# Optimization experiments

Hardware: AMD Instinct MI355X
Metric: run time of the kernel (lower is better)

Reference implementation:

```python
import jax, jax.numpy as jnp
import numpy as np

NUM_NODES = 100000
NUM_EDGES = 625000
IN_FEATURES = 128
OUT_FEATURES = 128


def setup_inputs() -> dict:
    key = jax.random.key(0)
    k1, k2, k3, k4 = jax.random.split(key, 4)
    x = jax.random.normal(k1, (NUM_NODES, IN_FEATURES), dtype=jnp.float32)
    edge_index = jax.random.randint(k2, (2, NUM_EDGES), 0, NUM_NODES, dtype=jnp.int64)
    # Xavier uniform for W (fan_in=IN, fan_out=OUT); B initialized to zeros in the
    # original, but we use small random values so gradients flow through both paths.
    limit = float(np.sqrt(6.0 / (IN_FEATURES + OUT_FEATURES)))
    W = jax.random.uniform(k3, (OUT_FEATURES, IN_FEATURES), dtype=jnp.float32,
                           minval=-limit, maxval=limit)
    B = jax.random.uniform(k4, (OUT_FEATURES, IN_FEATURES), dtype=jnp.float32,
                           minval=-limit, maxval=limit)
    return {"x": x, "edge_index": edge_index, "W": W, "B": B}


def reference(x, edge_index, W, B):
    sources, destinations = edge_index[0], edge_index[1]
    # message: gather destination features, scatter-add into source slots
    messages = x[destinations]                                        # [E, F_in]
    agg = jax.ops.segment_sum(messages, sources, num_segments=x.shape[0])  # [N, F_in]
    # in-degree (w.r.t. sources) normalization; zero-degree -> divide by 1
    deg = jax.ops.segment_sum(jnp.ones((sources.shape[0],), dtype=x.dtype),
                              sources, num_segments=x.shape[0])       # [N]
    deg = jnp.where(deg == 0, jnp.ones_like(deg), deg)
    agg = agg / deg[:, None]
    # update: (W @ messages.T + B @ x.T).T == messages @ W.T + x @ B.T
    out = agg @ W.T + x @ B.T                                         # [N, F_out]
    return out
```

## Files before the change

kernel.cpp:

```cpp
#include <hip/hip_runtime.h>

#define F_IN   128
#define F_OUT  128

typedef __attribute__((ext_vector_type(8))) short short8;
typedef __attribute__((ext_vector_type(4))) float floatx4;

__device__ __forceinline__ float bf16u_to_f_lo(unsigned int u) {
    union { unsigned int i; float f; } c; c.i = u << 16; return c.f;
}
__device__ __forceinline__ float bf16u_to_f_hi(unsigned int u) {
    union { unsigned int i; float f; } c; c.i = u & 0xffff0000u; return c.f;
}
__device__ __forceinline__ unsigned short f_to_bf16(float f) {
    union { float f; unsigned int i; } c; c.f = f;
    unsigned int u = c.i;
    u += 0x7fffu + ((u >> 16) & 1u);
    return (unsigned short)(u >> 16);
}
__device__ __forceinline__ unsigned int pack2(unsigned short a, unsigned short b) {
    return (unsigned int)a | ((unsigned int)b << 16);
}

__global__ void zero_kernel(int* __restrict__ p, long n) {
    long i = (long)blockIdx.x * blockDim.x + threadIdx.x;
    long stride = (long)gridDim.x * blockDim.x;
    for (; i < n; i += stride) p[i] = 0;
}

__global__ void hist_kernel(const int* __restrict__ src, int* __restrict__ cnt, int E) {
    int e = blockIdx.x * blockDim.x + threadIdx.x;
    if (e < E) atomicAdd(&cnt[src[e]], 1);
}

__global__ __launch_bounds__(256) void chunk_sums_kernel(const int* __restrict__ cnt,
                                                         int* __restrict__ partials, int n) {
    __shared__ int s[256];
    int b = blockIdx.x, t = threadIdx.x;
    int base = b * 1024 + t * 4;
    int sum = 0;
#pragma unroll
    for (int j = 0; j < 4; ++j) {
        int i = base + j;
        if (i < n) sum += cnt[i];
    }
    s[t] = sum;
    __syncthreads();
    for (int d = 128; d > 0; d >>= 1) {
        if (t < d) s[t] += s[t + d];
        __syncthreads();
    }
    if (t == 0) partials[b] = s[0];
}

__global__ __launch_bounds__(128) void scan_partials_kernel(const int* __restrict__ partials,
                                                            int* __restrict__ chunk_off, int nch) {
    __shared__ int s[128];
    int t = threadIdx.x;
    s[t] = (t < nch) ? partials[t] : 0;
    __syncthreads();
    for (int d = 1; d < 128; d <<= 1) {
        int val = s[t];
        int add = (t >= d) ? s[t - d] : 0;
        __syncthreads();
        s[t] = val + add;
        __syncthreads();
    }
    if (t < nch) chunk_off[t] = (t > 0) ? s[t - 1] : 0;
}

__global__ __launch_bounds__(256) void scan_chunks_kernel(int* __restrict__ off,
                                                          const int* __restrict__ chunk_off,
                                                          int n) {
    __shared__ int s[256];
    int b = blockIdx.x, t = threadIdx.x;
    int base = b * 1024 + t * 4;
    int v[4];
#pragma unroll
    for (int j = 0; j < 4; ++j) {
        int i = base + j;
        v[j] = (i < n) ? off[i] : 0;
    }
    int l1 = v[0], l2 = l1 + v[1], l3 = l2 + v[2], tot = l3 + v[3];
    s[t] = tot;
    __syncthreads();
    for (int d = 1; d < 256; d <<= 1) {
        int val = s[t];
        int add = (t >= d) ? s[t - d] : 0;
        __syncthreads();
        s[t] = val + add;
        __syncthreads();
    }
    int thr_excl = ((t > 0) ? s[t - 1] : 0) + chunk_off[b];
    if (base + 0 < n) off[base + 0] = thr_excl;
    if (base + 1 < n) off[base + 1] = thr_excl + l1;
    if (base + 2 < n) off[base + 2] = thr_excl + l2;
    if (base + 3 < n) off[base + 3] = thr_excl + l3;
}

__global__ void fill_kernel(const int* __restrict__ ei, int* __restrict__ off,
                            int* __restrict__ dst_sorted, int E) {
    int e = blockIdx.x * blockDim.x + threadIdx.x;
    if (e < E) {
        int s = ei[e];
        int d = ei[E + e];
        int p = atomicAdd(&off[s], 1);
        dst_sorted[p] = d;
    }
}

__global__ __launch_bounds__(256) void convert_x_kernel(const float* __restrict__ x,
                                                        char* __restrict__ outb, int N) {
    long tid = (long)blockIdx.x * blockDim.x + threadIdx.x;
    if (tid >= (long)N * 32) return;
    int row = (int)(tid >> 5);
    int seg = (int)(tid & 31);
    float4 v = *(const float4*)(x + (size_t)row * 128 + seg * 4);
    unsigned short r[4] = {f_to_bf16(v.x), f_to_bf16(v.y), f_to_bf16(v.z), f_to_bf16(v.w)};
    *(ushort4*)(outb + (size_t)row * 512 + 256 + seg * 8) =
        make_ushort4(r[0], r[1], r[2], r[3]);
}

__global__ __launch_bounds__(256) void gather_bf16_kernel(const int* __restrict__ off,
                                                          const int* __restrict__ dst_sorted,
                                                          char* __restrict__ outb, int N) {
    int node = blockIdx.x * 16 + (threadIdx.x >> 4);
    int lane = threadIdx.x & 15;
    if (node >= N) return;
    int start = (node == 0) ? 0 : off[node - 1];
    int end = off[node];
    float acc[8];
#pragma unroll
    for (int i = 0; i < 8; ++i) acc[i] = 0.0f;

    const char* xb = outb;
    int j = start;
    for (; j + 4 <= end; j += 4) {
        int d0 = dst_sorted[j];
        int d1 = dst_sorted[j + 1];
        int d2 = dst_sorted[j + 2];
        int d3 = dst_sorted[j + 3];
        uint4 a = *(const uint4*)(xb + (size_t)d0 * 512 + 256 + lane * 16);
        uint4 b = *(const uint4*)(xb + (size_t)d1 * 512 + 256 + lane * 16);
        uint4 c = *(const uint4*)(xb + (size_t)d2 * 512 + 256 + lane * 16);
        uint4 d = *(const uint4*)(xb + (size_t)d3 * 512 + 256 + lane * 16);
        acc[0] += bf16u_to_f_lo(a.x); acc[1] += bf16u_to_f_hi(a.x);
        acc[2] += bf16u_to_f_lo(a.y); acc[3] += bf16u_to_f_hi(a.y);
        acc[4] += bf16u_to_f_lo(a.z); acc[5] += bf16u_to_f_hi(a.z);
        acc[6] += bf16u_to_f_lo(a.w); acc[7] += bf16u_to_f_hi(a.w);
        acc[0] += bf16u_to_f_lo(b.x); acc[1] += bf16u_to_f_hi(b.x);
        acc[2] += bf16u_to_f_lo(b.y); acc[3] += bf16u_to_f_hi(b.y);
        acc[4] += bf16u_to_f_lo(b.z); acc[5] += bf16u_to_f_hi(b.z);
        acc[6] += bf16u_to_f_lo(b.w); acc[7] += bf16u_to_f_hi(b.w);
        acc[0] += bf16u_to_f_lo(c.x); acc[1] += bf16u_to_f_hi(c.x);
        acc[2] += bf16u_to_f_lo(c.y); acc[3] += bf16u_to_f_hi(c.y);
        acc[4] += bf16u_to_f_lo(c.z); acc[5] += bf16u_to_f_hi(c.z);
        acc[6] += bf16u_to_f_lo(c.w); acc[7] += bf16u_to_f_hi(c.w);
        acc[0] += bf16u_to_f_lo(d.x); acc[1] += bf16u_to_f_hi(d.x);
        acc[2] += bf16u_to_f_lo(d.y); acc[3] += bf16u_to_f_hi(d.y);
        acc[4] += bf16u_to_f_lo(d.z); acc[5] += bf16u_to_f_hi(d.z);
        acc[6] += bf16u_to_f_lo(d.w); acc[7] += bf16u_to_f_hi(d.w);
    }
    for (; j < end; ++j) {
        int d0 = dst_sorted[j];
        uint4 a = *(const uint4*)(xb + (size_t)d0 * 512 + 256 + lane * 16);
        acc[0] += bf16u_to_f_lo(a.x); acc[1] += bf16u_to_f_hi(a.x);
        acc[2] += bf16u_to_f_lo(a.y); acc[3] += bf16u_to_f_hi(a.y);
        acc[4] += bf16u_to_f_lo(a.z); acc[5] += bf16u_to_f_hi(a.z);
        acc[6] += bf16u_to_f_lo(a.w); acc[7] += bf16u_to_f_hi(a.w);
    }
    int deg = end - start;
    float scale = (deg > 0) ? (1.0f / (float)deg) : 1.0f;
    unsigned short r[8];
#pragma unroll
    for (int i = 0; i < 8; ++i) r[i] = f_to_bf16(acc[i] * scale);
    uint4 pk;
    pk.x = pack2(r[0], r[1]);
    pk.y = pack2(r[2], r[3]);
    pk.z = pack2(r[4], r[5]);
    pk.w = pack2(r[6], r[7]);
    *(uint4*)(outb + (size_t)node * 512 + lane * 16) = pk;
}

__global__ __launch_bounds__(256) void gemm_mfma_kernel(const float* __restrict__ W,
                                                        const float* __restrict__ Bm,
                                                        float* __restrict__ out, int N) {
    __shared__ uint4 Bs[4096];
    int t = threadIdx.x;
    int lane = t & 63;
    int w = t >> 6;
    int m16 = lane & 15;
    int quad = lane >> 4;

#pragma unroll
    for (int nt2 = 0; nt2 < 2; ++nt2) {
        int nt = w * 2 + nt2;
        int n = nt * 16 + m16;
#pragma unroll
        for (int s = 0; s < 8; ++s) {
            int kbase = s * 32 + quad * 8;
            const float* srcp = (kbase < 128) ? (W + n * 128 + kbase)
                                              : (Bm + n * 128 + (kbase - 128));
            float4 v0 = *(const float4*)srcp;
            float4 v1 = *(const float4*)(srcp + 4);
            uint4 pk;
            pk.x = pack2(f_to_bf16(v0.x), f_to_bf16(v0.y));
            pk.y = pack2(f_to_bf16(v0.z), f_to_bf16(v0.w));
            pk.z = pack2(f_to_bf16(v1.x), f_to_bf16(v1.y));
            pk.w = pack2(f_to_bf16(v1.z), f_to_bf16(v1.w));
            Bs[(nt * 8 + s) * 64 + lane] = pk;
        }
    }
    __syncthreads();

    int rowbase = blockIdx.x * 128 + w * 32;
    short8 afrag[2][8];
#pragma unroll
    for (int g = 0; g < 2; ++g) {
        int arow = rowbase + g * 16 + m16;
        if (arow > N - 1) arow = N - 1;
        const char* ab = (const char*)out + (size_t)arow * 512;
#pragma unroll
        for (int s = 0; s < 8; ++s)
            afrag[g][s] = *(const short8*)(ab + s * 64 + quad * 16);
    }

    floatx4 acc[2][8];
#pragma unroll
    for (int g = 0; g < 2; ++g)
#pragma unroll
        for (int nt = 0; nt < 8; ++nt) acc[g][nt] = (floatx4){0.f, 0.f, 0.f, 0.f};

#pragma unroll
    for (int nt = 0; nt < 8; ++nt) {
#pragma unroll
        for (int s = 0; s < 8; ++s) {
            short8 bfrag = *(const short8*)&Bs[(nt * 8 + s) * 64 + lane];
            acc[0][nt] = __builtin_amdgcn_mfma_f32_16x16x32_bf16(afrag[0][s], bfrag, acc[0][nt], 0, 0, 0);
            acc[1][nt] = __builtin_amdgcn_mfma_f32_16x16x32_bf16(afrag[1][s], bfrag, acc[1][nt], 0, 0, 0);
        }
    }

#pragma unroll
    for (int g = 0; g < 2; ++g)
#pragma unroll
        for (int nt = 0; nt < 8; ++nt)
#pragma unroll
            for (int r = 0; r < 4; ++r) {
                int gr = rowbase + g * 16 + quad * 4 + r;
                if (gr < N) out[(size_t)gr * 128 + nt * 16 + m16] = acc[g][nt][r];
            }
}

__global__ void invdeg_kernel(int* __restrict__ deg_io, int N) {
    int i = blockIdx.x * blockDim.x + threadIdx.x;
    if (i < N) {
        int d = deg_io[i];
        float inv = (d > 0) ? (1.0f / (float)d) : 1.0f;
        ((float*)deg_io)[i] = inv;
    }
}

__global__ __launch_bounds__(128) void scatter_atomic_kernel(const float* __restrict__ x,
                                                             const int* __restrict__ ei,
                                                             const float* __restrict__ invdeg,
                                                             float* __restrict__ out, int E) {
    int e = blockIdx.x;
    int f = threadIdx.x;
    int s = ei[e];
    int d = ei[E + e];
    float v = x[(long)d * F_IN + f] * invdeg[s];
    atomicAdd(&out[(long)s * F_IN + f], v);
}

__global__ __launch_bounds__(256) void gemm_fused_kernel(const float* __restrict__ x,
                                                         const float* __restrict__ W,
                                                         const float* __restrict__ Bm,
                                                         float* __restrict__ out, int N) {
    __shared__ float As[64][68];
    __shared__ float Ms[64][132];
    int t = threadIdx.x;
    int row0 = blockIdx.x * 64;
    int c0 = (t & 31) * 4;
    int r0 = (t >> 5) * 8;
    float acc[8][4];
#pragma unroll
    for (int i = 0; i < 8; ++i)
#pragma unroll
        for (int j = 0; j < 4; ++j) acc[i][j] = 0.0f;

    for (int kc = 0; kc < 4; ++kc) {
        const float* Asrc = (kc < 2) ? out : x;
        const float* Msrc = (kc < 2) ? W : Bm;
        int k0 = (kc & 1) * 64;
#pragma unroll
        for (int i = 0; i < 4; ++i) {
            int flat = t + 256 * i;
            int m = flat >> 4, ks = flat & 15;
            int row = row0 + m;
            float4 v = make_float4(0.f, 0.f, 0.f, 0.f);
            if (row < N) v = *(const float4*)&Asrc[(long)row * 128 + k0 + ks * 4];
            As[ks * 4 + 0][m] = v.x;
            As[ks * 4 + 1][m] = v.y;
            As[ks * 4 + 2][m] = v.z;
            As[ks * 4 + 3][m] = v.w;
        }
#pragma unroll
        for (int i = 0; i < 8; ++i) {
            int flat = t + 256 * i;
            int c = flat >> 4, ks = flat & 15;
            float4 v = *(const float4*)&Msrc[(long)c * 128 + k0 + ks * 4];
            Ms[ks * 4 + 0][c] = v.x;
            Ms[ks * 4 + 1][c] = v.y;
            Ms[ks * 4 + 2][c] = v.z;
            Ms[ks * 4 + 3][c] = v.w;
        }
        __syncthreads();
#pragma unroll 8
        for (int kk = 0; kk < 64; ++kk) {
            float4 a0 = *(const float4*)&As[kk][r0];
            float4 a1 = *(const float4*)&As[kk][r0 + 4];
            float4 m0 = *(const float4*)&Ms[kk][c0];
            float a[8] = {a0.x, a0.y, a0.z, a0.w, a1.x, a1.y, a1.z, a1.w};
            float m[4] = {m0.x, m0.y, m0.z, m0.w};
#pragma unroll
            for (int i = 0; i < 8; ++i)
#pragma unroll
                for (int j = 0; j < 4; ++j) acc[i][j] += a[i] * m[j];
        }
        __syncthreads();
    }
#pragma unroll
    for (int i = 0; i < 8; ++i) {
        int row = row0 + r0 + i;
        if (row < N) {
            float4 v = make_float4(acc[i][0], acc[i][1], acc[i][2], acc[i][3]);
            *(float4*)&out[(long)row * 128 + c0] = v;
        }
    }
}


extern "C" void kernel_launch(void* const* d_in, const int* in_sizes, int n_in,
                              void* d_out, int out_size, void* d_ws, size_t ws_size,
                              hipStream_t stream) {
    const float* x = (const float*)d_in[0];
    const int* ei = (const int*)d_in[1];
    const float* W = (const float*)d_in[2];
    const float* Bm = (const float*)d_in[3];
    float* out = (float*)d_out;

    const int N = in_sizes[0] / F_IN;
    const int E = in_sizes[1] / 2;
    const int NCHUNK = (N + 1023) / 1024;

    int* off        = (int*)d_ws;
    int* partials   = off + N;
    int* chunk_off  = partials + 128;
    int* dst_sorted = chunk_off + 128;

    const size_t need_csr = ((size_t)N + 256 + (size_t)E) * sizeof(int);
    const size_t need_deg = (size_t)N * sizeof(int);

    if (ws_size >= need_csr) {
        zero_kernel<<<256, 256, 0, stream>>>(off, N);
        hist_kernel<<<(E + 255) / 256, 256, 0, stream>>>(ei, off, E);
        chunk_sums_kernel<<<NCHUNK, 256, 0, stream>>>(off, partials, N);
        scan_partials_kernel<<<1, 128, 0, stream>>>(partials, chunk_off, NCHUNK);
        scan_chunks_kernel<<<NCHUNK, 256, 0, stream>>>(off, chunk_off, N);
        fill_kernel<<<(E + 255) / 256, 256, 0, stream>>>(ei, off, dst_sorted, E);
        {
            long tot = (long)N * 32;
            convert_x_kernel<<<(int)((tot + 255) / 256), 256, 0, stream>>>(x, (char*)out, N);
        }
        gather_bf16_kernel<<<(N + 15) / 16, 256, 0, stream>>>(off, dst_sorted, (char*)out, N);
        gemm_mfma_kernel<<<(N + 127) / 128, 256, 0, stream>>>(W, Bm, out, N);
    } else if (ws_size >= need_deg) {
        int* deg = (int*)d_ws;
        zero_kernel<<<256, 256, 0, stream>>>(deg, N);
        hist_kernel<<<(E + 255) / 256, 256, 0, stream>>>(ei, deg, E);
        invdeg_kernel<<<(N + 255) / 256, 256, 0, stream>>>(deg, N);
        zero_kernel<<<512, 256, 0, stream>>>((int*)out, (long)N * F_IN);
        scatter_atomic_kernel<<<E, 128, 0, stream>>>(x, ei, (const float*)deg, out, E);
        gemm_fused_kernel<<<(N + 63) / 64, 256, 0, stream>>>(x, W, Bm, out, N);
    }
}
```

Measured before the change: 232.8 us.

## Fuse neighbor gather into MFMA GEMM and merge x conversion with offset zeroing

Adds a fused path in which each GEMM block gathers and averages neighbor bf16 rows straight into MFMA A-fragments, so the aggregated features are never written to and re-read from global memory. The bf16 copy of x moves to a separate workspace buffer, and its conversion is merged with zeroing the offset array into one grid-stride prep kernel, removing two launches. In exchange, the gather now runs inside a GEMM block whose lanes each handle one node across four 64-byte strides, which may give less memory-level parallelism and more load imbalance than the old dedicated gather kernel. It also needs extra workspace, and the atomic fallback path is dropped.

```diff
diff --git a/kernel.cpp b/kernel.cpp
--- a/kernel.cpp
+++ b/kernel.cpp
@@ -21,11 +21,31 @@
 __device__ __forceinline__ unsigned int pack2(unsigned short a, unsigned short b) {
     return (unsigned int)a | ((unsigned int)b << 16);
 }
-
-__global__ void zero_kernel(int* __restrict__ p, long n) {
-    long i = (long)blockIdx.x * blockDim.x + threadIdx.x;
+__device__ __forceinline__ void acc8(float* a, uint4 v) {
+    a[0] += bf16u_to_f_lo(v.x); a[1] += bf16u_to_f_hi(v.x);
+    a[2] += bf16u_to_f_lo(v.y); a[3] += bf16u_to_f_hi(v.y);
+    a[4] += bf16u_to_f_lo(v.z); a[5] += bf16u_to_f_hi(v.z);
+    a[6] += bf16u_to_f_lo(v.w); a[7] += bf16u_to_f_hi(v.w);
+}
+
+__global__ __launch_bounds__(256) void prep_kernel(const float* __restrict__ x,
+                                                   int* __restrict__ off,
+                                                   unsigned short* __restrict__ xb, int N) {
+    long tid = (long)blockIdx.x * blockDim.x + threadIdx.x;
+    long nconv = (long)N * 32;
+    long total = nconv + N;
     long stride = (long)gridDim.x * blockDim.x;
-    for (; i < n; i += stride) p[i] = 0;
+    for (; tid < total; tid += stride) {
+        if (tid < nconv) {
+            int row = (int)(tid >> 5);
+            int seg = (int)(tid & 31);
+            float4 v = *(const float4*)(x + (size_t)row * 128 + seg * 4);
+            *(ushort4*)(xb + (size_t)row * 128 + seg * 4) =
+                make_ushort4(f_to_bf16(v.x), f_to_bf16(v.y), f_to_bf16(v.z), f_to_bf16(v.w));
+        } else {
+            off[tid - nconv] = 0;
+        }
+    }
 }
 
 __global__ void hist_kernel(const int* __restrict__ src, int* __restrict__ cnt, int E) {
@@ -109,82 +129,12 @@
     }
 }
 
-__global__ __launch_bounds__(256) void convert_x_kernel(const float* __restrict__ x,
-                                                        char* __restrict__ outb, int N) {
-    long tid = (long)blockIdx.x * blockDim.x + threadIdx.x;
-    if (tid >= (long)N * 32) return;
-    int row = (int)(tid >> 5);
-    int seg = (int)(tid & 31);
-    float4 v = *(const float4*)(x + (size_t)row * 128 + seg * 4);
-    unsigned short r[4] = {f_to_bf16(v.x), f_to_bf16(v.y), f_to_bf16(v.z), f_to_bf16(v.w)};
-    *(ushort4*)(outb + (size_t)row * 512 + 256 + seg * 8) =
-        make_ushort4(r[0], r[1], r[2], r[3]);
-}
-
-__global__ __launch_bounds__(256) void gather_bf16_kernel(const int* __restrict__ off,
+__global__ __launch_bounds__(256) void gather_gemm_kernel(const float* __restrict__ W,
+                                                          const float* __restrict__ Bm,
+                                                          const int* __restrict__ off,
                                                           const int* __restrict__ dst_sorted,
-                                                          char* __restrict__ outb, int N) {
-    int node = blockIdx.x * 16 + (threadIdx.x >> 4);
-    int lane = threadIdx.x & 15;
-    if (node >= N) return;
-    int start = (node == 0) ? 0 : off[node - 1];
-    int end = off[node];
-    float acc[8];
-#pragma unroll
-    for (int i = 0; i < 8; ++i) acc[i] = 0.0f;
-
-    const char* xb = outb;
-    int j = start;
-    for (; j + 4 <= end; j += 4) {
-        int d0 = dst_sorted[j];
-        int d1 = dst_sorted[j + 1];
-        int d2 = dst_sorted[j + 2];
-        int d3 = dst_sorted[j + 3];
-        uint4 a = *(const uint4*)(xb + (size_t)d0 * 512 + 256 + lane * 16);
-        uint4 b = *(const uint4*)(xb + (size_t)d1 * 512 + 256 + lane * 16);
-        uint4 c = *(const uint4*)(xb + (size_t)d2 * 512 + 256 + lane * 16);
-        uint4 d = *(const uint4*)(xb + (size_t)d3 * 512 + 256 + lane * 16);
-        acc[0] += bf16u_to_f_lo(a.x); acc[1] += bf16u_to_f_hi(a.x);
-        acc[2] += bf16u_to_f_lo(a.y); acc[3] += bf16u_to_f_hi(a.y);
-        acc[4] += bf16u_to_f_lo(a.z); acc[5] += bf16u_to_f_hi(a.z);
-        acc[6] += bf16u_to_f_lo(a.w); acc[7] += bf16u_to_f_hi(a.w);
-        acc[0] += bf16u_to_f_lo(b.x); acc[1] += bf16u_to_f_hi(b.x);
-        acc[2] += bf16u_to_f_lo(b.y); acc[3] += bf16u_to_f_hi(b.y);
-        acc[4] += bf16u_to_f_lo(b.z); acc[5] += bf16u_to_f_hi(b.z);
-        acc[6] += bf16u_to_f_lo(b.w); acc[7] += bf16u_to_f_hi(b.w);
-        acc[0] += bf16u_to_f_lo(c.x); acc[1] += bf16u_to_f_hi(c.x);
-        acc[2] += bf16u_to_f_lo(c.y); acc[3] += bf16u_to_f_hi(c.y);
-        acc[4] += bf16u_to_f_lo(c.z); acc[5] += bf16u_to_f_hi(c.z);
-        acc[6] += bf16u_to_f_lo(c.w); acc[7] += bf16u_to_f_hi(c.w);
-        acc[0] += bf16u_to_f_lo(d.x); acc[1] += bf16u_to_f_hi(d.x);
-        acc[2] += bf16u_to_f_lo(d.y); acc[3] += bf16u_to_f_hi(d.y);
-        acc[4] += bf16u_to_f_lo(d.z); acc[5] += bf16u_to_f_hi(d.z);
-        acc[6] += bf16u_to_f_lo(d.w); acc[7] += bf16u_to_f_hi(d.w);
-    }
-    for (; j < end; ++j) {
-        int d0 = dst_sorted[j];
-        uint4 a = *(const uint4*)(xb + (size_t)d0 * 512 + 256 + lane * 16);
-        acc[0] += bf16u_to_f_lo(a.x); acc[1] += bf16u_to_f_hi(a.x);
-        acc[2] += bf16u_to_f_lo(a.y); acc[3] += bf16u_to_f_hi(a.y);
-        acc[4] += bf16u_to_f_lo(a.z); acc[5] += bf16u_to_f_hi(a.z);
-        acc[6] += bf16u_to_f_lo(a.w); acc[7] += bf16u_to_f_hi(a.w);
-    }
-    int deg = end - start;
-    float scale = (deg > 0) ? (1.0f / (float)deg) : 1.0f;
-    unsigned short r[8];
-#pragma unroll
-    for (int i = 0; i < 8; ++i) r[i] = f_to_bf16(acc[i] * scale);
-    uint4 pk;
-    pk.x = pack2(r[0], r[1]);
-    pk.y = pack2(r[2], r[3]);
-    pk.z = pack2(r[4], r[5]);
-    pk.w = pack2(r[6], r[7]);
-    *(uint4*)(outb + (size_t)node * 512 + lane * 16) = pk;
-}
-
-__global__ __launch_bounds__(256) void gemm_mfma_kernel(const float* __restrict__ W,
-                                                        const float* __restrict__ Bm,
-                                                        float* __restrict__ out, int N) {
+                                                          const unsigned short* __restrict__ xb,
+                                                          float* __restrict__ out, int N) {
     __shared__ uint4 Bs[4096];
     int t = threadIdx.x;
     int lane = t & 63;
@@ -215,6 +165,175 @@
 
     int rowbase = blockIdx.x * 128 + w * 32;
     short8 afrag[2][8];
+
+#pragma unroll
+    for (int g = 0; g < 2; ++g) {
+        int node = rowbase + g * 16 + m16;
+        if (node > N - 1) node = N - 1;
+        int start = (node == 0) ? 0 : off[node - 1];
+        int end = off[node];
+        int deg = end - start;
+
+        float acc[4][8];
+#pragma unroll
+        for (int s = 0; s < 4; ++s)
+#pragma unroll
+            for (int j = 0; j < 8; ++j) acc[s][j] = 0.0f;
+
+        int j = start;
+        for (; j + 2 <= end; j += 2) {
+            int d0 = dst_sorted[j];
+            int d1 = dst_sorted[j + 1];
+            const char* p0 = (const char*)xb + (size_t)d0 * 256 + quad * 16;
+            const char* p1 = (const char*)xb + (size_t)d1 * 256 + quad * 16;
+            uint4 a0 = *(const uint4*)(p0);
+            uint4 a1 = *(const uint4*)(p0 + 64);
+            uint4 a2 = *(const uint4*)(p0 + 128);
+            uint4 a3 = *(const uint4*)(p0 + 192);
+            uint4 b0 = *(const uint4*)(p1);
+            uint4 b1 = *(const uint4*)(p1 + 64);
+            uint4 b2 = *(const uint4*)(p1 + 128);
+            uint4 b3 = *(const uint4*)(p1 + 192);
+            acc8(acc[0], a0); acc8(acc[1], a1); acc8(acc[2], a2); acc8(acc[3], a3);
+            acc8(acc[0], b0); acc8(acc[1], b1); acc8(acc[2], b2); acc8(acc[3], b3);
+        }
+        if (j < end) {
+            int d0 = dst_sorted[j];
+            const char* p0 = (const char*)xb + (size_t)d0 * 256 + quad * 16;
+            uint4 a0 = *(const uint4*)(p0);
+            uint4 a1 = *(const uint4*)(p0 + 64);
+            uint4 a2 = *(const uint4*)(p0 + 128);
+            uint4 a3 = *(const uint4*)(p0 + 192);
+            acc8(acc[0], a0); acc8(acc[1], a1); acc8(acc[2], a2); acc8(acc[3], a3);
+        }
+
+        float scale = (deg > 0) ? (1.0f / (float)deg) : 1.0f;
+#pragma unroll
+        for (int s = 0; s < 4; ++s) {
+            uint4 pk;
+            pk.x = pack2(f_to_bf16(acc[s][0] * scale), f_to_bf16(acc[s][1] * scale));
+            pk.y = pack2(f_to_bf16(acc[s][2] * scale), f_to_bf16(acc[s][3] * scale));
+            pk.z = pack2(f_to_bf16(acc[s][4] * scale), f_to_bf16(acc[s][5] * scale));
+            pk.w = pack2(f_to_bf16(acc[s][6] * scale), f_to_bf16(acc[s][7] * scale));
+            afrag[g][s] = *(short8*)&pk;
+        }
+        const char* q0 = (const char*)xb + (size_t)node * 256 + quad * 16;
+#pragma unroll
+        for (int s = 0; s < 4; ++s)
+            afrag[g][4 + s] = *(const short8*)(q0 + s * 64);
+    }
+
+    floatx4 acc[2][8];
+#pragma unroll
+    for (int g = 0; g < 2; ++g)
+#pragma unroll
+        for (int nt = 0; nt < 8; ++nt) acc[g][nt] = (floatx4){0.f, 0.f, 0.f, 0.f};
+
+#pragma unroll
+    for (int nt = 0; nt < 8; ++nt) {
+#pragma unroll
+        for (int s = 0; s < 8; ++s) {
+            short8 bfrag = *(const short8*)&Bs[(nt * 8 + s) * 64 + lane];
+            acc[0][nt] = __builtin_amdgcn_mfma_f32_16x16x32_bf16(afrag[0][s], bfrag, acc[0][nt], 0, 0, 0);
+            acc[1][nt] = __builtin_amdgcn_mfma_f32_16x16x32_bf16(afrag[1][s], bfrag, acc[1][nt], 0, 0, 0);
+        }
+    }
+
+#pragma unroll
+    for (int g = 0; g < 2; ++g)
+#pragma unroll
+        for (int nt = 0; nt < 8; ++nt)
+#pragma unroll
+            for (int r = 0; r < 4; ++r) {
+                int gr = rowbase + g * 16 + quad * 4 + r;
+                if (gr < N) out[(size_t)gr * 128 + nt * 16 + m16] = acc[g][nt][r];
+            }
+}
+
+__global__ void zero_kernel(int* __restrict__ p, long n) {
+    long i = (long)blockIdx.x * blockDim.x + threadIdx.x;
+    long stride = (long)gridDim.x * blockDim.x;
+    for (; i < n; i += stride) p[i] = 0;
+}
+
+__global__ __launch_bounds__(256) void convert_x_kernel(const float* __restrict__ x,
+                                                        char* __restrict__ outb, int N) {
+    long tid = (long)blockIdx.x * blockDim.x + threadIdx.x;
+    if (tid >= (long)N * 32) return;
+    int row = (int)(tid >> 5);
+    int seg = (int)(tid & 31);
+    float4 v = *(const float4*)(x + (size_t)row * 128 + seg * 4);
+    *(ushort4*)(outb + (size_t)row * 512 + 256 + seg * 8) =
+        make_ushort4(f_to_bf16(v.x), f_to_bf16(v.y), f_to_bf16(v.z), f_to_bf16(v.w));
+}
+
+__global__ __launch_bounds__(256) void gather_bf16_kernel(const int* __restrict__ off,
+                                                          const int* __restrict__ dst_sorted,
+                                                          char* __restrict__ outb, int N) {
+    int node = blockIdx.x * 16 + (threadIdx.x >> 4);
+    int lane = threadIdx.x & 15;
+    if (node >= N) return;
+    int start = (node == 0) ? 0 : off[node - 1];
+    int end = off[node];
+    float acc[8];
+#pragma unroll
+    for (int i = 0; i < 8; ++i) acc[i] = 0.0f;
+    const char* xb = outb;
+    int j = start;
+    for (; j + 2 <= end; j += 2) {
+        int d0 = dst_sorted[j];
+        int d1 = dst_sorted[j + 1];
+        uint4 a = *(const uint4*)(xb + (size_t)d0 * 512 + 256 + lane * 16);
+        uint4 b = *(const uint4*)(xb + (size_t)d1 * 512 + 256 + lane * 16);
+        acc8(acc, a); acc8(acc, b);
+    }
+    if (j < end) {
+        int d0 = dst_sorted[j];
+        uint4 a = *(const uint4*)(xb + (size_t)d0 * 512 + 256 + lane * 16);
+        acc8(acc, a);
+    }
+    int deg = end - start;
+    float scale = (deg > 0) ? (1.0f / (float)deg) : 1.0f;
+    uint4 pk;
+    pk.x = pack2(f_to_bf16(acc[0] * scale), f_to_bf16(acc[1] * scale));
+    pk.y = pack2(f_to_bf16(acc[2] * scale), f_to_bf16(acc[3] * scale));
+    pk.z = pack2(f_to_bf16(acc[4] * scale), f_to_bf16(acc[5] * scale));
+    pk.w = pack2(f_to_bf16(acc[6] * scale), f_to_bf16(acc[7] * scale));
+    *(uint4*)(outb + (size_t)node * 512 + lane * 16) = pk;
+}
+
+__global__ __launch_bounds__(256) void gemm_mfma_kernel(const float* __restrict__ W,
+                                                        const float* __restrict__ Bm,
+                                                        float* __restrict__ out, int N) {
+    __shared__ uint4 Bs[4096];
+    int t = threadIdx.x;
+    int lane = t & 63;
+    int w = t >> 6;
+    int m16 = lane & 15;
+    int quad = lane >> 4;
+#pragma unroll
+    for (int nt2 = 0; nt2 < 2; ++nt2) {
+        int nt = w * 2 + nt2;
+        int n = nt * 16 + m16;
+#pragma unroll
+        for (int s = 0; s < 8; ++s) {
+            int kbase = s * 32 + quad * 8;
+            const float* srcp = (kbase < 128) ? (W + n * 128 + kbase)
+                                              : (Bm + n * 128 + (kbase - 128));
+            float4 v0 = *(const float4*)srcp;
+            float4 v1 = *(const float4*)(srcp + 4);
+            uint4 pk;
+            pk.x = pack2(f_to_bf16(v0.x), f_to_bf16(v0.y));
+            pk.y = pack2(f_to_bf16(v0.z), f_to_bf16(v0.w));
+            pk.z = pack2(f_to_bf16(v1.x), f_to_bf16(v1.y));
+            pk.w = pack2(f_to_bf16(v1.z), f_to_bf16(v1.w));
+            Bs[(nt * 8 + s) * 64 + lane] = pk;
+        }
+    }
+    __syncthreads();
+
+    int rowbase = blockIdx.x * 128 + w * 32;
+    short8 afrag[2][8];
 #pragma unroll
     for (int g = 0; g < 2; ++g) {
         int arow = rowbase + g * 16 + m16;
@@ -240,7 +359,6 @@
             acc[1][nt] = __builtin_amdgcn_mfma_f32_16x16x32_bf16(afrag[1][s], bfrag, acc[1][nt], 0, 0, 0);
         }
     }
-
 #pragma unroll
     for (int g = 0; g < 2; ++g)
 #pragma unroll
@@ -250,94 +368,6 @@
                 int gr = rowbase + g * 16 + quad * 4 + r;
                 if (gr < N) out[(size_t)gr * 128 + nt * 16 + m16] = acc[g][nt][r];
             }
-}
-
-__global__ void invdeg_kernel(int* __restrict__ deg_io, int N) {
-    int i = blockIdx.x * blockDim.x + threadIdx.x;
-    if (i < N) {
-        int d = deg_io[i];
-        float inv = (d > 0) ? (1.0f / (float)d) : 1.0f;
-        ((float*)deg_io)[i] = inv;
-    }
-}
-
-__global__ __launch_bounds__(128) void scatter_atomic_kernel(const float* __restrict__ x,
-                                                             const int* __restrict__ ei,
-                                                             const float* __restrict__ invdeg,
-                                                             float* __restrict__ out, int E) {
-    int e = blockIdx.x;
-    int f = threadIdx.x;
-    int s = ei[e];
-    int d = ei[E + e];
-    float v = x[(long)d * F_IN + f] * invdeg[s];
-    atomicAdd(&out[(long)s * F_IN + f], v);
-}
-
-__global__ __launch_bounds__(256) void gemm_fused_kernel(const float* __restrict__ x,
-                                                         const float* __restrict__ W,
-                                                         const float* __restrict__ Bm,
-                                                         float* __restrict__ out, int N) {
-    __shared__ float As[64][68];
-    __shared__ float Ms[64][132];
-    int t = threadIdx.x;
-    int row0 = blockIdx.x * 64;
-    int c0 = (t & 31) * 4;
-    int r0 = (t >> 5) * 8;
-    float acc[8][4];
-#pragma unroll
-    for (int i = 0; i < 8; ++i)
-#pragma unroll
-        for (int j = 0; j < 4; ++j) acc[i][j] = 0.0f;
-
-    for (int kc = 0; kc < 4; ++kc) {
-        const float* Asrc = (kc < 2) ? out : x;
-        const float* Msrc = (kc < 2) ? W : Bm;
-        int k0 = (kc & 1) * 64;
-#pragma unroll
-        for (int i = 0; i < 4; ++i) {
-            int flat = t + 256 * i;
-            int m = flat >> 4, ks = flat & 15;
-            int row = row0 + m;
-            float4 v = make_float4(0.f, 0.f, 0.f, 0.f);
-            if (row < N) v = *(const float4*)&Asrc[(long)row * 128 + k0 + ks * 4];
-            As[ks * 4 + 0][m] = v.x;
-            As[ks * 4 + 1][m] = v.y;
-            As[ks * 4 + 2][m] = v.z;
-            As[ks * 4 + 3][m] = v.w;
-        }
-#pragma unroll
-        for (int i = 0; i < 8; ++i) {
-            int flat = t + 256 * i;
-            int c = flat >> 4, ks = flat & 15;
-            float4 v = *(const float4*)&Msrc[(long)c * 128 + k0 + ks * 4];
-            Ms[ks * 4 + 0][c] = v.x;
-            Ms[ks * 4 + 1][c] = v.y;
-            Ms[ks * 4 + 2][c] = v.z;
-            Ms[ks * 4 + 3][c] = v.w;
-        }
-        __syncthreads();
-#pragma unroll 8
-        for (int kk = 0; kk < 64; ++kk) {
-            float4 a0 = *(const float4*)&As[kk][r0];
-            float4 a1 = *(const float4*)&As[kk][r0 + 4];
-            float4 m0 = *(const float4*)&Ms[kk][c0];
-            float a[8] = {a0.x, a0.y, a0.z, a0.w, a1.x, a1.y, a1.z, a1.w};
-            float m[4] = {m0.x, m0.y, m0.z, m0.w};
-#pragma unroll
-            for (int i = 0; i < 8; ++i)
-#pragma unroll
-                for (int j = 0; j < 4; ++j) acc[i][j] += a[i] * m[j];
-        }
-        __syncthreads();
-    }
-#pragma unroll
-    for (int i = 0; i < 8; ++i) {
-        int row = row0 + r0 + i;
-        if (row < N) {
-            float4 v = make_float4(acc[i][0], acc[i][1], acc[i][2], acc[i][3]);
-            *(float4*)&out[(long)row * 128 + c0] = v;
-        }
-    }
 }
 
 
@@ -358,11 +388,21 @@
     int* partials   = off + N;
     int* chunk_off  = partials + 128;
     int* dst_sorted = chunk_off + 128;
-
-    const size_t need_csr = ((size_t)N + 256 + (size_t)E) * sizeof(int);
-    const size_t need_deg = (size_t)N * sizeof(int);
-
-    if (ws_size >= need_csr) {
+    size_t xb_off   = (((size_t)(N + 256 + E) * sizeof(int)) + 255) & ~(size_t)255;
+    unsigned short* xb = (unsigned short*)((char*)d_ws + xb_off);
+
+    const size_t need_fused = xb_off + (size_t)N * 128 * sizeof(unsigned short);
+    const size_t need_csr   = ((size_t)N + 256 + (size_t)E) * sizeof(int);
+
+    if (ws_size >= need_fused) {
+        prep_kernel<<<512, 256, 0, stream>>>(x, off, xb, N);
+        hist_kernel<<<(E + 255) / 256, 256, 0, stream>>>(ei, off, E);
+        chunk_sums_kernel<<<NCHUNK, 256, 0, stream>>>(off, partials, N);
+        scan_partials_kernel<<<1, 128, 0, stream>>>(partials, chunk_off, NCHUNK);
+        scan_chunks_kernel<<<NCHUNK, 256, 0, stream>>>(off, chunk_off, N);
+        fill_kernel<<<(E + 255) / 256, 256, 0, stream>>>(ei, off, dst_sorted, E);
+        gather_gemm_kernel<<<(N + 127) / 128, 256, 0, stream>>>(W, Bm, off, dst_sorted, xb, out, N);
+    } else if (ws_size >= need_csr) {
         zero_kernel<<<256, 256, 0, stream>>>(off, N);
         hist_kernel<<<(E + 255) / 256, 256, 0, stream>>>(ei, off, E);
         chunk_sums_kernel<<<NCHUNK, 256, 0, stream>>>(off, partials, N);
@@ -375,13 +415,5 @@
         }
         gather_bf16_kernel<<<(N + 15) / 16, 256, 0, stream>>>(off, dst_sorted, (char*)out, N);
         gemm_mfma_kernel<<<(N + 127) / 128, 256, 0, stream>>>(W, Bm, out, N);
-    } else if (ws_size >= need_deg) {
-        int* deg = (int*)d_ws;
-        zero_kernel<<<256, 256, 0, stream>>>(deg, N);
-        hist_kernel<<<(E + 255) / 256, 256, 0, stream>>>(ei, deg, E);
-        invdeg_kernel<<<(N + 255) / 256, 256, 0, stream>>>(deg, N);
-        zero_kernel<<<512, 256, 0, stream>>>((int*)out, (long)N * F_IN);
-        scatter_atomic_kernel<<<E, 128, 0, stream>>>(x, ei, (const float*)deg, out, E);
-        gemm_fused_kernel<<<(N + 63) / 64, 256, 0, stream>>>(x, W, Bm, out, N);
-    }
-}
+    }
+}
```

New measurement: 238.5 us. 1.02x slower.
